# Performance work log

Measured on AMD Instinct MI355X. Metric: run time of the kernel, lower is better.

The kernel has to match this reference:

```python
import jax, jax.numpy as jnp
import numpy as np

# hyperparams matching init_kwargs
T_LEN = 1024
T_LATENCY = 7
TB = T_LATENCY + 1          # t_len_block
N_OUT = 1024
BATCH = 32
FS_SCALE = 10.0             # FastSigmoid default scale


@jax.custom_vjp
def fast_sigmoid(x):
    # forward: Heaviside; backward: fast-sigmoid surrogate
    return (x > 0).astype(x.dtype)

def _fs_fwd(x):
    return (x > 0).astype(x.dtype), x

def _fs_bwd(x, g):
    return (g / (FS_SCALE * jnp.abs(x) + 1.0) ** 2,)

fast_sigmoid.defvjp(_fs_fwd, _fs_bwd)


def setup_inputs() -> dict:
    key = jax.random.key(0)
    k1, k2, k3, k4 = jax.random.split(key, 4)
    x = jax.random.normal(k1, (T_LEN, BATCH, N_OUT), dtype=jnp.float32) * 0.6
    # raw params; forward applies the clamp/abs 'properties' of the module
    beta_raw = jax.random.uniform(k2, (N_OUT,), minval=0.7, maxval=0.99, dtype=jnp.float32)
    p_raw = jax.random.uniform(k3, (N_OUT,), minval=0.5, maxval=0.95, dtype=jnp.float32)
    b_raw = jax.random.uniform(k4, (N_OUT,), minval=0.2, maxval=1.0, dtype=jnp.float32)
    return {"x": x, "beta_raw": beta_raw, "p_raw": p_raw, "b_raw": b_raw}


def reference(x, beta_raw, p_raw, b_raw):
    T, B, N = x.shape
    tb = TB
    n_blocks = T // tb  # t_pad == 0 by construction
    dt = x.dtype

    # clamped properties
    beta = jnp.clip(beta_raw, 0.001, 0.999)          # [N]
    p = jnp.clip(jnp.abs(p_raw), 0.0, 0.999)         # [N]
    bb = jnp.clip(jnp.abs(b_raw), 0.001, 1.0)        # [N]

    t_idx = jnp.arange(tb)
    expo = t_idx[:, None] - t_idx[None, :]            # [tb,tb], t - s
    lower = expo >= 0
    # causal decay kernel: beta^(t-s) for s<=t  (grouped conv1d equivalent)
    beta_pow = jnp.where(lower[:, :, None],
                         beta[None, None, :] ** jnp.maximum(expo, 0)[:, :, None].astype(dt),
                         jnp.zeros((), dt))           # [tb,tb,N]
    # phi kernel: weight (t-s+1) for s<=t  (conv2d equivalent)
    phi = jnp.where(lower, (expo + 1).astype(dt), jnp.zeros((), dt))  # [tb,tb]
    p_exp = jnp.arange(1, tb + 1, dtype=dt)           # [tb]
    p_pow = p[None, :] ** p_exp[:, None]              # [tb,N]
    inv_p = 1.0 / p                                   # [N]

    def body(carry, x_slice):
        spikes, z, int_mem, a_kernel = carry          # [tb,B,N],[tb,B,N],[B,N],[tb,B,N]
        sg = jax.lax.stop_gradient(spikes)            # detach_spike_grad=True
        maskf = (jnp.max(sg, axis=0) > 0).astype(dt)  # [B,N] any spike in prev block
        # refractory masking of input
        xs = jnp.where(z < maskf[None], jnp.zeros((), dt), x_slice)
        v_init = int_mem * (1.0 - maskf)
        # adaptation update
        a_at_spike = jnp.sum(a_kernel * sg, axis=0) + inv_p          # [B,N]
        decay_steps = jnp.sum(z > 1, axis=0).astype(dt)              # [B,N]
        new_a = a_at_spike * jnp.power(p[None, :], decay_steps)
        a = a_kernel[-1] * (1.0 - maskf) + new_a * maskf             # [B,N]
        a_k = p_pow[:, None, :] * a[None]                             # [tb,B,N]
        v_th = 1.0 + bb[None, None, :] * a_k                          # [tb,B,N]
        # --- Block forward ---
        cur = xs.at[0].add(beta[None, :] * v_init)
        membrane = jnp.einsum('tsn,sbn->tbn', beta_pow, cur)          # causal decayed sum
        faulty = fast_sigmoid(membrane - v_th)                        # [tb,B,N] 0/1
        z_new = jnp.einsum('ts,sbn->tbn', phi, faulty)
        # g(): keep only entries exactly 1, straight-through grad
        spikes_new = z_new - jax.lax.stop_gradient(
            jnp.where(z_new == 1.0, jnp.zeros((), dt), z_new))
        return (spikes_new, z_new, membrane[-1], a_k), spikes_new

    z0 = jnp.zeros((tb, B, N), dt)
    carry0 = (z0, z0, jnp.zeros((B, N), dt), z0)
    xb = x.reshape(n_blocks, tb, B, N)
    _, out = jax.lax.scan(body, carry0, xb)
    return out.reshape(T, B, N)
```

## Files before the change

kernel.cpp:

```cpp
#include <hip/hip_runtime.h>


constexpr int T_LEN = 1024;
constexpr int TB    = 8;
constexpr int NBLK  = T_LEN / TB;
constexpr int BATCH = 32;
constexpr int NOUT  = 1024;
constexpr int BN    = BATCH * NOUT;
constexpr int RING  = 8;

typedef float f4 __attribute__((ext_vector_type(4)));

template <int N>  struct ic { static constexpr int  value = N; };
template <bool B> struct bc { static constexpr bool value = B; };

__device__ __forceinline__ void dma16(const float* g, float* l) {
    __builtin_amdgcn_global_load_lds(
        (const __attribute__((address_space(1))) void*)g,
        (__attribute__((address_space(3))) void*)l, 16, 0, 0);
}

__global__ __launch_bounds__(128, 1)
void snn_blocks_kernel(const float* __restrict__ x,
                       const float* __restrict__ beta_raw,
                       const float* __restrict__ p_raw,
                       const float* __restrict__ b_raw,
                       float* __restrict__ out)
{
    __shared__ float inbuf[RING][TB * 64];
    __shared__ float sbuf[2][TB * 64];

    const int tid  = threadIdx.x;
    const int lane = tid & 63;
    const int wid  = tid >> 6;
    const int wg0  = blockIdx.x * 64;

    if (wid == 1) {
        const int rowoff = lane >> 4;
        const int coloff = wg0 + (lane & 15) * 4;
        const float* xbase = x   + (ptrdiff_t)rowoff * BN + coloff;
        float*       obase = out + (ptrdiff_t)rowoff * BN + coloff;

#pragma unroll
        for (int k = 0; k < RING - 1; ++k) {
            const float* g = xbase + (ptrdiff_t)(k * TB) * BN;
            dma16(g,          &inbuf[k][0]);
            dma16(g + 4 * BN, &inbuf[k][256]);
        }
        asm volatile("s_waitcnt vmcnt(12)" ::: "memory");
        __builtin_amdgcn_s_barrier();

        auto piter = [&](auto Wt, int k, auto Dr, auto Dm) {
            constexpr int  W     = decltype(Wt)::value;
            constexpr bool drain = decltype(Dr)::value;
            constexpr bool dma   = decltype(Dm)::value;
            __builtin_amdgcn_sched_barrier(0);
            if constexpr (drain) {
                const float* sf = &sbuf[(k - 1) & 1][0];
                f4 s0 = *(const f4*)(sf + lane * 4);
                f4 s1 = *(const f4*)(sf + 256 + lane * 4);
                *(f4*)(obase + (ptrdiff_t)((k - 1) * TB) * BN)     = s0;
                *(f4*)(obase + (ptrdiff_t)((k - 1) * TB + 4) * BN) = s1;
            }
            __builtin_amdgcn_sched_barrier(0);
            if constexpr (dma) {
                const float* g = xbase + (ptrdiff_t)((k + 7) * TB) * BN;
                float* l = &inbuf[(k + 7) & 7][0];
                dma16(g,          l);
                dma16(g + 4 * BN, l + 256);
            }
            __builtin_amdgcn_sched_barrier(0);
            if constexpr (W >= 0)
                asm volatile("s_waitcnt vmcnt(%0)" :: "i"(W) : "memory");
            __builtin_amdgcn_s_barrier();
        };

        piter(ic<12>{}, 0, bc<false>{}, bc<true>{});
        piter(ic<14>{}, 1, bc<true>{},  bc<true>{});
        piter(ic<16>{}, 2, bc<true>{},  bc<true>{});
        piter(ic<18>{}, 3, bc<true>{},  bc<true>{});
        piter(ic<20>{}, 4, bc<true>{},  bc<true>{});
        piter(ic<22>{}, 5, bc<true>{},  bc<true>{});
#pragma unroll 1
        for (int k = 6; k <= 120; ++k)
            piter(ic<24>{}, k, bc<true>{}, bc<true>{});
        piter(ic<22>{}, 121, bc<true>{}, bc<false>{});
        piter(ic<20>{}, 122, bc<true>{}, bc<false>{});
        piter(ic<18>{}, 123, bc<true>{}, bc<false>{});
        piter(ic<16>{}, 124, bc<true>{}, bc<false>{});
        piter(ic<14>{}, 125, bc<true>{}, bc<false>{});
        piter(ic<12>{}, 126, bc<true>{}, bc<false>{});
        piter(ic<-1>{}, 127, bc<true>{}, bc<false>{});

        {
            const float* sf = &sbuf[1][0];
            f4 s0 = *(const f4*)(sf + lane * 4);
            f4 s1 = *(const f4*)(sf + 256 + lane * 4);
            *(f4*)(obase + (ptrdiff_t)(127 * TB) * BN)     = s0;
            *(f4*)(obase + (ptrdiff_t)(127 * TB + 4) * BN) = s1;
        }
    } else {
        const int gid = wg0 + lane;
        const int n   = gid & (NOUT - 1);

        double beta = (double)beta_raw[n];
        beta = beta < 0.001 ? 0.001 : (beta > 0.999 ? 0.999 : beta);
        double p = fabs((double)p_raw[n]);
        p = p > 0.999 ? 0.999 : p;
        double bb = fabs((double)b_raw[n]);
        bb = bb < 0.001 ? 0.001 : (bb > 1.0 ? 1.0 : bb);
        const double inv_p = 1.0 / p;

        double ppow[9];
        ppow[0] = 1.0;
#pragma unroll
        for (int i = 1; i <= 8; ++i) ppow[i] = ppow[i - 1] * p;
        double bbp[8];
#pragma unroll
        for (int t = 0; t < 8; ++t) bbp[t] = bb * ppow[t + 1];
        const double pp2 = ppow[2], pp4 = ppow[4], pp8 = ppow[8];

        double m = 0.0, a = 0.0;
        int maskf = 0, firstp = 0;

        __builtin_amdgcn_s_barrier();

#pragma unroll 1
        for (int k = 0; k < NBLK; ++k) {
            __builtin_amdgcn_sched_barrier(0);
            const int slot = k & 7;
            float cur[8];
#pragma unroll
            for (int t = 0; t < 8; ++t) cur[t] = inbuf[slot][t * 64 + lane];

            double pf1 = p;
            pf1 *= (firstp & 1) ? p   : 1.0;
            pf1 *= (firstp & 2) ? pp2 : 1.0;
            pf1 *= (firstp & 4) ? pp4 : 1.0;
            const int dsteps = firstp ^ 7;
            double pd = (dsteps & 1) ? p : 1.0;
            pd *= (dsteps & 2) ? pp2 : 1.0;
            pd *= (dsteps & 4) ? pp4 : 1.0;
            const double new_a = (a * pf1 + inv_p) * pd;
            double vinit;
            if (maskf) { a = new_a;   vinit = 0.0; }
            else       { a = pp8 * a; vinit = m;   }

            const int zmask = maskf ? ((1 << firstp) - 1) : 0;

            int fbits = 0;
            double mm = vinit;
#pragma unroll
            for (int t = 0; t < 8; ++t) {
                const float xf = ((zmask >> t) & 1) ? 0.0f : cur[t];
                mm = beta * mm + (double)xf;
                const double vth = 1.0 + bbp[t] * a;
                fbits |= (mm - vth > 0.0) ? (1 << t) : 0;
            }
            m = mm;
            maskf  = (fbits != 0);
            firstp = fbits ? __builtin_ctz(fbits) : 0;

#pragma unroll
            for (int t = 0; t < 8; ++t)
                sbuf[k & 1][t * 64 + lane] =
                    (maskf && t == firstp) ? 1.0f : 0.0f;

            asm volatile("s_waitcnt lgkmcnt(0)" ::: "memory");
            __builtin_amdgcn_s_barrier();
        }
    }
}

extern "C" void kernel_launch(void* const* d_in, const int* in_sizes, int n_in,
                              void* d_out, int out_size, void* d_ws, size_t ws_size,
                              hipStream_t stream) {
    const float* x        = (const float*)d_in[0];
    const float* beta_raw = (const float*)d_in[1];
    const float* p_raw    = (const float*)d_in[2];
    const float* b_raw    = (const float*)d_in[3];
    float* out            = (float*)d_out;

    dim3 grid(BN / 64);
    dim3 block(128);
    snn_blocks_kernel<<<grid, block, 0, stream>>>(x, beta_raw, p_raw, b_raw, out);
}
```

Measured before the change: 232.7 us.

## Batch four time blocks per producer/consumer barrier with larger LDS ring

Restructures the warp-specialized pipeline so each barrier round covers four time blocks instead of one. The ring grows to 16 slots and the output staging buffer to two groups of four. This cuts the number of workgroup barriers and waitcnt stalls between the DMA warp and the compute warp by a factor of four. In exchange it uses more LDS, makes the prefetch depth coarser, and issues larger bursts of loads and stores per round.

```diff
diff --git a/kernel.cpp b/kernel.cpp
--- a/kernel.cpp
+++ b/kernel.cpp
@@ -7,12 +7,11 @@
 constexpr int BATCH = 32;
 constexpr int NOUT  = 1024;
 constexpr int BN    = BATCH * NOUT;
-constexpr int RING  = 8;
+constexpr int G     = 4;
+constexpr int NITER = NBLK / G;
+constexpr int RING  = 16;
 
 typedef float f4 __attribute__((ext_vector_type(4)));
-
-template <int N>  struct ic { static constexpr int  value = N; };
-template <bool B> struct bc { static constexpr bool value = B; };
 
 __device__ __forceinline__ void dma16(const float* g, float* l) {
     __builtin_amdgcn_global_load_lds(
@@ -28,7 +27,7 @@
                        float* __restrict__ out)
 {
     __shared__ float inbuf[RING][TB * 64];
-    __shared__ float sbuf[2][TB * 64];
+    __shared__ float sbuf[2][G][TB * 64];
 
     const int tid  = threadIdx.x;
     const int lane = tid & 63;
@@ -41,64 +40,58 @@
         const float* xbase = x   + (ptrdiff_t)rowoff * BN + coloff;
         float*       obase = out + (ptrdiff_t)rowoff * BN + coloff;
 
+        auto dmaGroup = [&](int j2) {
 #pragma unroll
-        for (int k = 0; k < RING - 1; ++k) {
-            const float* g = xbase + (ptrdiff_t)(k * TB) * BN;
-            dma16(g,          &inbuf[k][0]);
-            dma16(g + 4 * BN, &inbuf[k][256]);
-        }
-        asm volatile("s_waitcnt vmcnt(12)" ::: "memory");
-        __builtin_amdgcn_s_barrier();
-
-        auto piter = [&](auto Wt, int k, auto Dr, auto Dm) {
-            constexpr int  W     = decltype(Wt)::value;
-            constexpr bool drain = decltype(Dr)::value;
-            constexpr bool dma   = decltype(Dm)::value;
-            __builtin_amdgcn_sched_barrier(0);
-            if constexpr (drain) {
-                const float* sf = &sbuf[(k - 1) & 1][0];
-                f4 s0 = *(const f4*)(sf + lane * 4);
-                f4 s1 = *(const f4*)(sf + 256 + lane * 4);
-                *(f4*)(obase + (ptrdiff_t)((k - 1) * TB) * BN)     = s0;
-                *(f4*)(obase + (ptrdiff_t)((k - 1) * TB + 4) * BN) = s1;
-            }
-            __builtin_amdgcn_sched_barrier(0);
-            if constexpr (dma) {
-                const float* g = xbase + (ptrdiff_t)((k + 7) * TB) * BN;
-                float* l = &inbuf[(k + 7) & 7][0];
+            for (int i = 0; i < G; ++i) {
+                const int b = j2 * G + i;
+                const float* g = xbase + (ptrdiff_t)(b * TB) * BN;
+                float* l = &inbuf[b & (RING - 1)][0];
                 dma16(g,          l);
                 dma16(g + 4 * BN, l + 256);
             }
-            __builtin_amdgcn_sched_barrier(0);
-            if constexpr (W >= 0)
-                asm volatile("s_waitcnt vmcnt(%0)" :: "i"(W) : "memory");
-            __builtin_amdgcn_s_barrier();
+        };
+        auto drainIter = [&](int j) {
+#pragma unroll
+            for (int i = 0; i < G; ++i) {
+                const float* sf = &sbuf[j & 1][i][0];
+                f4 s0 = *(const f4*)(sf + lane * 4);
+                f4 s1 = *(const f4*)(sf + 256 + lane * 4);
+                const int b = j * G + i;
+                *(f4*)(obase + (ptrdiff_t)(b * TB) * BN)     = s0;
+                *(f4*)(obase + (ptrdiff_t)(b * TB + 4) * BN) = s1;
+            }
         };
 
-        piter(ic<12>{}, 0, bc<false>{}, bc<true>{});
-        piter(ic<14>{}, 1, bc<true>{},  bc<true>{});
-        piter(ic<16>{}, 2, bc<true>{},  bc<true>{});
-        piter(ic<18>{}, 3, bc<true>{},  bc<true>{});
-        piter(ic<20>{}, 4, bc<true>{},  bc<true>{});
-        piter(ic<22>{}, 5, bc<true>{},  bc<true>{});
+        dmaGroup(0);
+        dmaGroup(1);
+        asm volatile("s_waitcnt vmcnt(8)" ::: "memory");
+        __builtin_amdgcn_s_barrier();
+        asm volatile("" ::: "memory");
+
+        dmaGroup(2);
+        asm volatile("s_waitcnt vmcnt(8)" ::: "memory");
+        __builtin_amdgcn_s_barrier();
+        asm volatile("" ::: "memory");
+
 #pragma unroll 1
-        for (int k = 6; k <= 120; ++k)
-            piter(ic<24>{}, k, bc<true>{}, bc<true>{});
-        piter(ic<22>{}, 121, bc<true>{}, bc<false>{});
-        piter(ic<20>{}, 122, bc<true>{}, bc<false>{});
-        piter(ic<18>{}, 123, bc<true>{}, bc<false>{});
-        piter(ic<16>{}, 124, bc<true>{}, bc<false>{});
-        piter(ic<14>{}, 125, bc<true>{}, bc<false>{});
-        piter(ic<12>{}, 126, bc<true>{}, bc<false>{});
-        piter(ic<-1>{}, 127, bc<true>{}, bc<false>{});
+        for (int j = 1; j <= 29; ++j) {
+            drainIter(j - 1);
+            dmaGroup(j + 2);
+            asm volatile("s_waitcnt vmcnt(16)" ::: "memory");
+            __builtin_amdgcn_s_barrier();
+            asm volatile("" ::: "memory");
+        }
 
-        {
-            const float* sf = &sbuf[1][0];
-            f4 s0 = *(const f4*)(sf + lane * 4);
-            f4 s1 = *(const f4*)(sf + 256 + lane * 4);
-            *(f4*)(obase + (ptrdiff_t)(127 * TB) * BN)     = s0;
-            *(f4*)(obase + (ptrdiff_t)(127 * TB + 4) * BN) = s1;
-        }
+        drainIter(29);
+        asm volatile("s_waitcnt vmcnt(8)" ::: "memory");
+        __builtin_amdgcn_s_barrier();
+        asm volatile("" ::: "memory");
+
+        drainIter(30);
+        __builtin_amdgcn_s_barrier();
+        asm volatile("" ::: "memory");
+
+        drainIter(31);
     } else {
         const int gid = wg0 + lane;
         const int n   = gid & (NOUT - 1);
@@ -124,50 +117,56 @@
         int maskf = 0, firstp = 0;
 
         __builtin_amdgcn_s_barrier();
+        asm volatile("" ::: "memory");
 
 #pragma unroll 1
-        for (int k = 0; k < NBLK; ++k) {
-            __builtin_amdgcn_sched_barrier(0);
-            const int slot = k & 7;
-            float cur[8];
-#pragma unroll
-            for (int t = 0; t < 8; ++t) cur[t] = inbuf[slot][t * 64 + lane];
-
-            double pf1 = p;
-            pf1 *= (firstp & 1) ? p   : 1.0;
-            pf1 *= (firstp & 2) ? pp2 : 1.0;
-            pf1 *= (firstp & 4) ? pp4 : 1.0;
-            const int dsteps = firstp ^ 7;
-            double pd = (dsteps & 1) ? p : 1.0;
-            pd *= (dsteps & 2) ? pp2 : 1.0;
-            pd *= (dsteps & 4) ? pp4 : 1.0;
-            const double new_a = (a * pf1 + inv_p) * pd;
-            double vinit;
-            if (maskf) { a = new_a;   vinit = 0.0; }
-            else       { a = pp8 * a; vinit = m;   }
-
-            const int zmask = maskf ? ((1 << firstp) - 1) : 0;
-
-            int fbits = 0;
-            double mm = vinit;
-#pragma unroll
-            for (int t = 0; t < 8; ++t) {
-                const float xf = ((zmask >> t) & 1) ? 0.0f : cur[t];
-                mm = beta * mm + (double)xf;
-                const double vth = 1.0 + bbp[t] * a;
-                fbits |= (mm - vth > 0.0) ? (1 << t) : 0;
-            }
-            m = mm;
-            maskf  = (fbits != 0);
-            firstp = fbits ? __builtin_ctz(fbits) : 0;
+        for (int j = 0; j < NITER; ++j) {
+            const int g0 = (j & 3) * G;
 
 #pragma unroll
-            for (int t = 0; t < 8; ++t)
-                sbuf[k & 1][t * 64 + lane] =
-                    (maskf && t == firstp) ? 1.0f : 0.0f;
+            for (int i = 0; i < G; ++i) {
+                float cur[8];
+#pragma unroll
+                for (int t = 0; t < 8; ++t)
+                    cur[t] = inbuf[g0 + i][t * 64 + lane];
+
+                double pf1 = p;
+                pf1 *= (firstp & 1) ? p   : 1.0;
+                pf1 *= (firstp & 2) ? pp2 : 1.0;
+                pf1 *= (firstp & 4) ? pp4 : 1.0;
+                const int dsteps = firstp ^ 7;
+                double pd = (dsteps & 1) ? p : 1.0;
+                pd *= (dsteps & 2) ? pp2 : 1.0;
+                pd *= (dsteps & 4) ? pp4 : 1.0;
+                const double new_a = (a * pf1 + inv_p) * pd;
+                double vinit;
+                if (maskf) { a = new_a;   vinit = 0.0; }
+                else       { a = pp8 * a; vinit = m;   }
+
+                const int zmask = maskf ? ((1 << firstp) - 1) : 0;
+
+                int fbits = 0;
+                double mm = vinit;
+#pragma unroll
+                for (int t = 0; t < 8; ++t) {
+                    const float xf = ((zmask >> t) & 1) ? 0.0f : cur[t];
+                    mm = beta * mm + (double)xf;
+                    const double vth = 1.0 + bbp[t] * a;
+                    fbits |= (mm - vth > 0.0) ? (1 << t) : 0;
+                }
+                m = mm;
+                maskf  = (fbits != 0);
+                firstp = fbits ? __builtin_ctz(fbits) : 0;
+
+#pragma unroll
+                for (int t = 0; t < 8; ++t)
+                    sbuf[j & 1][i][t * 64 + lane] =
+                        (maskf && t == firstp) ? 1.0f : 0.0f;
+            }
 
             asm volatile("s_waitcnt lgkmcnt(0)" ::: "memory");
             __builtin_amdgcn_s_barrier();
+            asm volatile("" ::: "memory");
         }
     }
 }
```

Result: no change. 237.3 us (+2.0%).
